# Kernel tuning notes

Hardware: AMD Instinct MI355X
Metric: run time of the kernel (lower is better)

The kernel has to match this reference:

```python
import jax, jax.numpy as jnp
import numpy as np

PI = 3.14159  # constant used in the torch module
N_QUBITS = 10
N_LAYERS = 4
B = 1024  # number of graphs


def _lin_init(k, fan_in, fan_out):
    k1, k2 = jax.random.split(k)
    s = 1.0 / np.sqrt(fan_in)
    W = jax.random.uniform(k1, (fan_in, fan_out), jnp.float32, -s, s)
    b = jax.random.uniform(k2, (fan_out,), jnp.float32, -s, s)
    return W, b


def setup_inputs():
    key = jax.random.key(0)
    ks = jax.random.split(key, 12)
    N, E, Fin, H, Emb = 32768, 131072, 128, 256, 128
    x = jax.random.normal(ks[0], (N, Fin), jnp.float32)
    edge_index = jax.random.randint(ks[1], (2, E), 0, N)
    batch = jnp.sort(jax.random.randint(ks[2], (N,), 0, B))
    edge_attr = jax.random.uniform(ks[3], (E, 4), dtype=jnp.float32)
    W1, b1 = _lin_init(ks[4], Fin, H)          # GCNConv 1
    W2, b2 = _lin_init(ks[5], H, Emb)          # GCNConv 2
    projW, projb = _lin_init(ks[6], Emb, N_QUBITS)
    vqc_weights = jax.random.uniform(ks[7], (N_LAYERS, N_QUBITS), jnp.float32, 0.0, 2 * np.pi)
    epW, epb = _lin_init(ks[8], 4, N_QUBITS - 1)
    cW1, cb1 = _lin_init(ks[9], Emb + N_QUBITS, 16)
    cW2, cb2 = _lin_init(ks[10], 16, 1)
    return dict(x=x, edge_index=edge_index, batch=batch, edge_attr=edge_attr,
                W1=W1, b1=b1, W2=W2, b2=b2, projW=projW, projb=projb,
                vqc_weights=vqc_weights, epW=epW, epb=epb,
                cW1=cW1, cb1=cb1, cW2=cW2, cb2=cb2)


def _gcn_conv(x, W, b, src, dst, n):
    # GCNConv with self-loops: sym-normalized aggregation of xW
    h = x @ W
    deg = jnp.zeros((n,), x.dtype).at[dst].add(1.0) + 1.0  # +1 self-loop
    dinv = jax.lax.rsqrt(deg)
    coef = (dinv[src] * dinv[dst])[:, None]
    agg = jnp.zeros_like(h).at[dst].add(h[src] * coef)
    return agg + h * (1.0 / deg)[:, None] + b


def _segment_mean(v, seg, n):
    tot = jnp.zeros((n, v.shape[1]), v.dtype).at[seg].add(v)
    cnt = jnp.zeros((n,), v.dtype).at[seg].add(1.0)
    return tot / jnp.clip(cnt, 1.0)[:, None]


def _run_vqc(q_in, weights, ep):
    # Batched real state-vector simulation. All gates (RY, CRY) are real.
    # Wire 0 = most significant bit (pennylane default.qubit convention).
    b = q_in.shape[0]
    dim = 2 ** N_QUBITS
    st = jnp.zeros((b, dim), q_in.dtype).at[:, 0].set(1.0)

    def ry(st, theta, w):
        th = jnp.broadcast_to(theta, (b,)) * 0.5
        c = jnp.cos(th)[:, None, None]
        s = jnp.sin(th)[:, None, None]
        r = st.reshape(b, 2 ** w, 2, -1)
        a0, a1 = r[:, :, 0], r[:, :, 1]
        return jnp.stack([c * a0 - s * a1, s * a0 + c * a1], axis=2).reshape(b, dim)

    def cry(st, theta, w):
        # control w, target w+1 (adjacent wires)
        th = jnp.broadcast_to(theta, (b,)) * 0.5
        c = jnp.cos(th)[:, None, None]
        s = jnp.sin(th)[:, None, None]
        r = st.reshape(b, 2 ** w, 2, 2, -1)
        a0, a1 = r[:, :, 1, 0], r[:, :, 1, 1]
        r = r.at[:, :, 1, 0].set(c * a0 - s * a1).at[:, :, 1, 1].set(s * a0 + c * a1)
        return r.reshape(b, dim)

    for i in range(N_QUBITS):                      # AngleEmbedding (RY)
        st = ry(st, q_in[:, i], i)
    for layer in range(N_LAYERS):
        for i in range(N_QUBITS):
            st = ry(st, weights[layer, i], i)
        for i in range(N_QUBITS - 1):
            st = cry(st, ep[:, i], i)

    probs = st * st
    zs = []
    for i in range(N_QUBITS):
        p = probs.reshape(b, 2 ** i, 2, -1).sum(axis=(1, 3))
        zs.append(p[:, 0] - p[:, 1])               # <PauliZ(i)>
    return jnp.stack(zs, axis=1)                   # [B, n_qubits]


def reference(x, edge_index, batch, edge_attr, W1, b1, W2, b2, projW, projb,
              vqc_weights, epW, epb, cW1, cb1, cW2, cb2):
    N = x.shape[0]
    src, dst = edge_index[0], edge_index[1]
    # GCN encoder: two GCNConv + ReLU, global mean pool (dropout = eval mode)
    h = jax.nn.relu(_gcn_conv(x, W1, b1, src, dst, N))
    h = jax.nn.relu(_gcn_conv(h, W2, b2, src, dst, N))
    emb = _segment_mean(h, batch, B)               # [B, gcn_embed]

    q_in = jnp.tanh(emb @ projW + projb) * PI      # [B, n_qubits]

    # scatter-mean edge pooling per graph, then edge projection
    edge_batch = batch[src]
    pooled_edge = _segment_mean(edge_attr, edge_batch, B)  # [B, 4]
    ep = pooled_edge @ epW + epb                   # [B, n_qubits-1]

    q_out = _run_vqc(q_in, vqc_weights, ep)        # [B, n_qubits]

    combined = jnp.concatenate([emb, q_out], axis=-1)
    hid = jax.nn.relu(combined @ cW1 + cb1)
    return hid @ cW2 + cb2                         # [B, num_tasks]
```

## Files before the change

kernel.cpp:

```cpp
#include <hip/hip_runtime.h>

#define PI_F 3.14159f
#define NQ 10

__global__ void k_edge_setup(const int* __restrict__ dstA, const int* __restrict__ srcA,
                             const int* __restrict__ batch, const float* __restrict__ eattr,
                             int E, int* __restrict__ cnt, float* __restrict__ psum,
                             float* __restrict__ ecnt) {
  int e = blockIdx.x * blockDim.x + threadIdx.x;
  if (e >= E) return;
  atomicAdd(&cnt[dstA[e]], 1);
  int g = batch[srcA[e]];
  float4 v = *(const float4*)(eattr + (size_t)e * 4);
  atomicAdd(&psum[g * 4 + 0], v.x);
  atomicAdd(&psum[g * 4 + 1], v.y);
  atomicAdd(&psum[g * 4 + 2], v.z);
  atomicAdd(&psum[g * 4 + 3], v.w);
  atomicAdd(&ecnt[g], 1.0f);
}

__global__ __launch_bounds__(1024) void k_scan1(const int* __restrict__ cnt,
                                                int* __restrict__ incl,
                                                int* __restrict__ bsum) {
  __shared__ int buf[1024];
  int t = threadIdx.x;
  int base = blockIdx.x << 10;
  buf[t] = cnt[base + t];
  __syncthreads();
#pragma unroll
  for (int off = 1; off < 1024; off <<= 1) {
    int x = (t >= off) ? buf[t - off] : 0;
    __syncthreads();
    buf[t] += x;
    __syncthreads();
  }
  incl[base + t] = buf[t];
  if (t == 1023) bsum[blockIdx.x] = buf[t];
}

__global__ void k_scan2(int* __restrict__ bsum, int nb) {
  int t = threadIdx.x;
  int v = (t < nb) ? bsum[t] : 0;
  int orig = v;
#pragma unroll
  for (int off = 1; off < 64; off <<= 1) {
    int x = __shfl_up(v, off, 64);
    if (t >= off) v += x;
  }
  if (t < nb) bsum[t] = v - orig;
}

__global__ void k_node_setup(const int* __restrict__ cnt, const int* __restrict__ incl,
                             const int* __restrict__ bsum, const int* __restrict__ batch,
                             int N, int Bn, int* __restrict__ rowStart,
                             int* __restrict__ pos, float* __restrict__ dinv,
                             float* __restrict__ invdeg, int* __restrict__ starts) {
  int i = blockIdx.x * blockDim.x + threadIdx.x;
  if (i >= N) return;
  int c = cnt[i];
  int inc = incl[i] + bsum[i >> 10];
  rowStart[i + 1] = inc;
  pos[i] = inc - c;
  if (i == 0) rowStart[0] = 0;
  float d = (float)c + 1.0f;
  dinv[i] = 1.0f / sqrtf(d);
  invdeg[i] = 1.0f / d;
  int b = batch[i];
  int bp = (i == 0) ? -1 : batch[i - 1];
  for (int g = bp + 1; g <= b; g++) starts[g] = i;
  if (i == N - 1) {
    for (int g = b + 1; g <= Bn; g++) starts[g] = N;
  }
}

__global__ void k_fill(const int* __restrict__ dst, int E, int* __restrict__ pos,
                       int* __restrict__ eSorted) {
  int e = blockIdx.x * blockDim.x + threadIdx.x;
  if (e < E) { int s = atomicAdd(&pos[dst[e]], 1); eSorted[s] = e; }
}

__global__ __launch_bounds__(256) void k_gemm(const float* __restrict__ A,
                                              const float* __restrict__ B,
                                              float* __restrict__ C,
                                              int M, int K, int N) {
  __shared__ float As[64][36];
  __shared__ float Bs[32][68];
  int t = threadIdx.x;
  int tx = t & 15, ty = t >> 4;
  int row0 = blockIdx.y * 64, col0 = blockIdx.x * 64;
  float acc[4][4] = {};
  for (int k0 = 0; k0 < K; k0 += 32) {
#pragma unroll
    for (int rep = 0; rep < 2; rep++) {
      int slot = t + rep * 256;
      int r = slot >> 3;
      int cg = (slot & 7) << 2;
      float4 v = *(const float4*)(A + (size_t)(row0 + r) * K + (k0 + cg));
      *(float4*)&As[r][cg] = v;
      int r2 = slot >> 4;
      int cg2 = (slot & 15) << 2;
      float4 w = *(const float4*)(B + (size_t)(k0 + r2) * N + (col0 + cg2));
      *(float4*)&Bs[r2][cg2] = w;
    }
    __syncthreads();
#pragma unroll
    for (int kk = 0; kk < 32; kk++) {
      float av[4];
      av[0] = As[ty * 4 + 0][kk];
      av[1] = As[ty * 4 + 1][kk];
      av[2] = As[ty * 4 + 2][kk];
      av[3] = As[ty * 4 + 3][kk];
      float4 b4 = *(const float4*)&Bs[kk][tx << 2];
      float bv[4] = {b4.x, b4.y, b4.z, b4.w};
#pragma unroll
      for (int i = 0; i < 4; i++)
#pragma unroll
        for (int j = 0; j < 4; j++) acc[i][j] = fmaf(av[i], bv[j], acc[i][j]);
    }
    __syncthreads();
  }
#pragma unroll
  for (int i = 0; i < 4; i++) {
    float4 v = {acc[i][0], acc[i][1], acc[i][2], acc[i][3]};
    *(float4*)(C + (size_t)(row0 + ty * 4 + i) * N + (col0 + (tx << 2))) = v;
  }
}

__global__ __launch_bounds__(256) void k_gcn_combine(
    const float* __restrict__ hlin, const int* __restrict__ srcA,
    const int* __restrict__ rowStart, const int* __restrict__ eSorted,
    const float* __restrict__ dinv, const float* __restrict__ invdeg,
    const float* __restrict__ bias, float* __restrict__ hout, int N, int C, int shift) {
  int gid = blockIdx.x * blockDim.x + threadIdx.x;
  int n = gid >> shift;
  if (n >= N) return;
  int cq = (gid & ((1 << shift) - 1)) << 2;
  int e0 = rowStart[n], e1 = rowStart[n + 1];
  float di = dinv[n];
  float ax = 0.f, ay = 0.f, az = 0.f, aw = 0.f;
  for (int e = e0; e < e1; e++) {
    int eidx = eSorted[e];
    int s = srcA[eidx];
    float coef = dinv[s] * di;
    float4 v = *(const float4*)(hlin + (size_t)s * C + cq);
    ax = fmaf(coef, v.x, ax);
    ay = fmaf(coef, v.y, ay);
    az = fmaf(coef, v.z, az);
    aw = fmaf(coef, v.w, aw);
  }
  float idg = invdeg[n];
  float4 hv = *(const float4*)(hlin + (size_t)n * C + cq);
  float4 bv = *(const float4*)(bias + cq);
  float4 r;
  r.x = fmaxf(fmaf(hv.x, idg, ax) + bv.x, 0.f);
  r.y = fmaxf(fmaf(hv.y, idg, ay) + bv.y, 0.f);
  r.z = fmaxf(fmaf(hv.z, idg, az) + bv.z, 0.f);
  r.w = fmaxf(fmaf(hv.w, idg, aw) + bv.w, 0.f);
  *(float4*)(hout + (size_t)n * C + cq) = r;
}

__device__ __forceinline__ void apply_ry(float* st, int w, float c, float s, int t) {
  int str = 1 << (9 - w);
#pragma unroll
  for (int r = 0; r < 2; r++) {
    int p = t + 256 * r;
    int lo = p & (str - 1);
    int hi = p >> (9 - w);
    int a0 = (hi << (10 - w)) + lo;
    int a1 = a0 + str;
    float x0 = st[a0], x1 = st[a1];
    st[a0] = c * x0 - s * x1;
    st[a1] = s * x0 + c * x1;
  }
}

__device__ __forceinline__ void apply_cry(float* st, int w, float c, float s, int t) {
  int ts = 1 << (8 - w);
  int lo = t & (ts - 1);
  int hi = t >> (8 - w);
  int a0 = (hi << (10 - w)) + (ts << 1) + lo;
  int a1 = a0 + ts;
  float x0 = st[a0], x1 = st[a1];
  st[a0] = c * x0 - s * x1;
  st[a1] = s * x0 + c * x1;
}

__global__ __launch_bounds__(256) void k_vqc_head(
    const float* __restrict__ h2, const int* __restrict__ starts,
    const float* __restrict__ psum, const float* __restrict__ ecnt,
    const float* __restrict__ projW, const float* __restrict__ projb,
    const float* __restrict__ vqcW, const float* __restrict__ epW,
    const float* __restrict__ epb, const float* __restrict__ cW1,
    const float* __restrict__ cb1, const float* __restrict__ cW2,
    const float* __restrict__ cb2, float* __restrict__ out) {
  int g = blockIdx.x;
  int t = threadIdx.x;
  __shared__ float st[1024];
  __shared__ float emb[128];
  __shared__ float csc[59], css[59];
  __shared__ float zred[4][NQ];
  __shared__ float zq[NQ];
  __shared__ float hid[16];

  int s0 = starts[g], s1 = starts[g + 1];
  int cntn = s1 - s0;
  float invc = 1.0f / (float)(cntn > 0 ? cntn : 1);
  if (t < 128) {
    float sum = 0.f;
    for (int i = s0; i < s1; i++) sum += h2[(size_t)i * 128 + t];
    emb[t] = sum * invc;
  }
  st[t] = 0.f; st[t + 256] = 0.f; st[t + 512] = 0.f; st[t + 768] = 0.f;
  __syncthreads();

  if (t < NQ) {
    float sum = projb[t];
    for (int k = 0; k < 128; k++) sum = fmaf(emb[k], projW[k * NQ + t], sum);
    float th = tanhf(sum) * PI_F * 0.5f;
    csc[t] = cosf(th);
    css[t] = sinf(th);
  } else if (t < NQ + 40) {
    float th = vqcW[t - NQ] * 0.5f;
    csc[t] = cosf(th);
    css[t] = sinf(th);
  } else if (t < 59) {
    int i = t - 50;
    float icnt = 1.0f / fmaxf(ecnt[g], 1.0f);
    float sum = epb[i];
    for (int j = 0; j < 4; j++) sum = fmaf(psum[g * 4 + j] * icnt, epW[j * 9 + i], sum);
    float th = sum * 0.5f;
    csc[t] = cosf(th);
    css[t] = sinf(th);
  }
  if (t == 0) st[0] = 1.0f;
  __syncthreads();

  for (int i = 0; i < NQ; i++) {
    apply_ry(st, i, csc[i], css[i], t);
    __syncthreads();
  }
  for (int L = 0; L < 4; L++) {
    for (int i = 0; i < NQ; i++) {
      apply_ry(st, i, csc[10 + L * 10 + i], css[10 + L * 10 + i], t);
      __syncthreads();
    }
    for (int i = 0; i < NQ - 1; i++) {
      apply_cry(st, i, csc[50 + i], css[50 + i], t);
      __syncthreads();
    }
  }

  float z[NQ];
#pragma unroll
  for (int i = 0; i < NQ; i++) z[i] = 0.f;
#pragma unroll
  for (int r = 0; r < 4; r++) {
    int a = t + 256 * r;
    float p = st[a] * st[a];
#pragma unroll
    for (int i = 0; i < NQ; i++) z[i] += ((a >> (9 - i)) & 1) ? -p : p;
  }
#pragma unroll
  for (int off = 32; off >= 1; off >>= 1) {
#pragma unroll
    for (int i = 0; i < NQ; i++) z[i] += __shfl_down(z[i], off, 64);
  }
  int wave = t >> 6, lane = t & 63;
  if (lane == 0) {
#pragma unroll
    for (int i = 0; i < NQ; i++) zred[wave][i] = z[i];
  }
  __syncthreads();
  if (t < NQ) zq[t] = zred[0][t] + zred[1][t] + zred[2][t] + zred[3][t];
  __syncthreads();

  if (t < 16) {
    float sum = cb1[t];
    for (int k = 0; k < 128; k++) sum = fmaf(emb[k], cW1[k * 16 + t], sum);
    for (int k = 0; k < NQ; k++) sum = fmaf(zq[k], cW1[(128 + k) * 16 + t], sum);
    hid[t] = fmaxf(sum, 0.f);
  }
  __syncthreads();
  if (t == 0) {
    float sum = cb2[0];
    for (int j = 0; j < 16; j++) sum = fmaf(hid[j], cW2[j], sum);
    out[g] = sum;
  }
}

extern "C" void kernel_launch(void* const* d_in, const int* in_sizes, int n_in,
                              void* d_out, int out_size, void* d_ws, size_t ws_size,
                              hipStream_t stream) {
  const float* x = (const float*)d_in[0];
  const int* ei = (const int*)d_in[1];
  const int* batch = (const int*)d_in[2];
  const float* eattr = (const float*)d_in[3];
  const float* W1 = (const float*)d_in[4];
  const float* b1 = (const float*)d_in[5];
  const float* W2 = (const float*)d_in[6];
  const float* b2 = (const float*)d_in[7];
  const float* projW = (const float*)d_in[8];
  const float* projb = (const float*)d_in[9];
  const float* vqcW = (const float*)d_in[10];
  const float* epW = (const float*)d_in[11];
  const float* epb = (const float*)d_in[12];
  const float* cW1 = (const float*)d_in[13];
  const float* cb1 = (const float*)d_in[14];
  const float* cW2 = (const float*)d_in[15];
  const float* cb2 = (const float*)d_in[16];
  float* out = (float*)d_out;

  const int N = in_sizes[0] / 128;
  const int E = in_sizes[1] / 2;
  const int Bn = out_size;

  const int* srcA = ei;
  const int* dstA = ei + E;

  char* ws = (char*)d_ws;
  float* bufA = (float*)ws;
  float* bufB = (float*)(ws + ((size_t)32 << 20));
  size_t off = (size_t)64 << 20;
  auto alloc = [&](size_t bytes) {
    size_t o = off;
    off += (bytes + 255) & ~(size_t)255;
    return o;
  };
  int* cnt = (int*)(ws + alloc((size_t)N * 4));
  float* psum = (float*)(ws + alloc((size_t)Bn * 4 * 4));
  float* ecnt = (float*)(ws + alloc((size_t)Bn * 4));
  size_t zeroEnd = off;
  int* rowStart = (int*)(ws + alloc((size_t)(N + 1) * 4));
  int* pos = (int*)(ws + alloc((size_t)N * 4));
  int* eSorted = (int*)(ws + alloc((size_t)E * 4));
  float* dinv = (float*)(ws + alloc((size_t)N * 4));
  float* invdeg = (float*)(ws + alloc((size_t)N * 4));
  int* starts = (int*)(ws + alloc((size_t)(Bn + 1) * 4));
  int* incl = (int*)(ws + alloc((size_t)N * 4));
  int* bsum = (int*)(ws + alloc(64 * 4));

  hipMemsetAsync(ws + ((size_t)64 << 20), 0, zeroEnd - ((size_t)64 << 20), stream);

  int eblocks = (E + 255) / 256;
  int nblocks = (N + 255) / 256;
  int nb1024 = N >> 10;

  k_edge_setup<<<eblocks, 256, 0, stream>>>(dstA, srcA, batch, eattr, E, cnt, psum, ecnt);
  k_scan1<<<nb1024, 1024, 0, stream>>>(cnt, incl, bsum);
  k_scan2<<<1, 64, 0, stream>>>(bsum, nb1024);
  k_node_setup<<<nblocks, 256, 0, stream>>>(cnt, incl, bsum, batch, N, Bn, rowStart, pos,
                                            dinv, invdeg, starts);
  k_fill<<<eblocks, 256, 0, stream>>>(dstA, E, pos, eSorted);

  {
    dim3 grid(256 / 64, N / 64);
    k_gemm<<<grid, 256, 0, stream>>>(x, W1, bufA, N, 128, 256);
  }
  k_gcn_combine<<<(N * 64) / 256, 256, 0, stream>>>(bufA, srcA, rowStart, eSorted, dinv,
                                                    invdeg, b1, bufB, N, 256, 6);
  {
    dim3 grid(128 / 64, N / 64);
    k_gemm<<<grid, 256, 0, stream>>>(bufB, W2, bufA, N, 256, 128);
  }
  k_gcn_combine<<<(N * 32) / 256, 256, 0, stream>>>(bufA, srcA, rowStart, eSorted, dinv,
                                                    invdeg, b2, bufB, N, 128, 5);
  k_vqc_head<<<Bn, 256, 0, stream>>>(bufB, starts, psum, ecnt, projW, projb, vqcW, epW,
                                     epb, cW1, cb1, cW2, cb2, out);
}
```

Baseline: 236.2 us.

## Pre-gather source ids and coefficients into CSR, pool edge attrs per node

The edge fill step now writes the source index and its dinv directly into dst-sorted arrays. The aggregation loop therefore no longer does the double indirection eSorted→srcA→dinv. Edge attributes are accumulated per source node rather than per graph, which spreads the atomics that used to hit 1024 hot addresses, and the head kernel reduces them per graph using a spare wavefront. The separate block-sum scan kernel is removed and each thread sums the preceding block totals itself. In exchange the zeroed workspace grows (N×20 bytes) and there is extra per-graph reduction work.

Measured after the change: 209.2 us. 1.13x faster.

```diff
diff --git a/kernel.cpp b/kernel.cpp
--- a/kernel.cpp
+++ b/kernel.cpp
@@ -4,19 +4,19 @@
 #define NQ 10
 
 __global__ void k_edge_setup(const int* __restrict__ dstA, const int* __restrict__ srcA,
-                             const int* __restrict__ batch, const float* __restrict__ eattr,
-                             int E, int* __restrict__ cnt, float* __restrict__ psum,
-                             float* __restrict__ ecnt) {
+                             const float* __restrict__ eattr, int E,
+                             int* __restrict__ cnt, float* __restrict__ nsum4,
+                             float* __restrict__ necnt) {
   int e = blockIdx.x * blockDim.x + threadIdx.x;
   if (e >= E) return;
   atomicAdd(&cnt[dstA[e]], 1);
-  int g = batch[srcA[e]];
+  int s = srcA[e];
   float4 v = *(const float4*)(eattr + (size_t)e * 4);
-  atomicAdd(&psum[g * 4 + 0], v.x);
-  atomicAdd(&psum[g * 4 + 1], v.y);
-  atomicAdd(&psum[g * 4 + 2], v.z);
-  atomicAdd(&psum[g * 4 + 3], v.w);
-  atomicAdd(&ecnt[g], 1.0f);
+  atomicAdd(&nsum4[(size_t)s * 4 + 0], v.x);
+  atomicAdd(&nsum4[(size_t)s * 4 + 1], v.y);
+  atomicAdd(&nsum4[(size_t)s * 4 + 2], v.z);
+  atomicAdd(&nsum4[(size_t)s * 4 + 3], v.w);
+  atomicAdd(&necnt[s], 1.0f);
 }
 
 __global__ __launch_bounds__(1024) void k_scan1(const int* __restrict__ cnt,
@@ -38,18 +38,6 @@
   if (t == 1023) bsum[blockIdx.x] = buf[t];
 }
 
-__global__ void k_scan2(int* __restrict__ bsum, int nb) {
-  int t = threadIdx.x;
-  int v = (t < nb) ? bsum[t] : 0;
-  int orig = v;
-#pragma unroll
-  for (int off = 1; off < 64; off <<= 1) {
-    int x = __shfl_up(v, off, 64);
-    if (t >= off) v += x;
-  }
-  if (t < nb) bsum[t] = v - orig;
-}
-
 __global__ void k_node_setup(const int* __restrict__ cnt, const int* __restrict__ incl,
                              const int* __restrict__ bsum, const int* __restrict__ batch,
                              int N, int Bn, int* __restrict__ rowStart,
@@ -57,8 +45,11 @@
                              float* __restrict__ invdeg, int* __restrict__ starts) {
   int i = blockIdx.x * blockDim.x + threadIdx.x;
   if (i >= N) return;
+  int blk = i >> 10;
+  int pre = 0;
+  for (int j = 0; j < blk; j++) pre += bsum[j];
   int c = cnt[i];
-  int inc = incl[i] + bsum[i >> 10];
+  int inc = incl[i] + pre;
   rowStart[i + 1] = inc;
   pos[i] = inc - c;
   if (i == 0) rowStart[0] = 0;
@@ -73,10 +64,15 @@
   }
 }
 
-__global__ void k_fill(const int* __restrict__ dst, int E, int* __restrict__ pos,
-                       int* __restrict__ eSorted) {
+__global__ void k_fill(const int* __restrict__ dst, const int* __restrict__ srcA,
+                       const float* __restrict__ dinv, int E, int* __restrict__ pos,
+                       int* __restrict__ srcSorted, float* __restrict__ dcoef) {
   int e = blockIdx.x * blockDim.x + threadIdx.x;
-  if (e < E) { int s = atomicAdd(&pos[dst[e]], 1); eSorted[s] = e; }
+  if (e >= E) return;
+  int s = srcA[e];
+  int slot = atomicAdd(&pos[dst[e]], 1);
+  srcSorted[slot] = s;
+  dcoef[slot] = dinv[s];
 }
 
 __global__ __launch_bounds__(256) void k_gemm(const float* __restrict__ A,
@@ -127,8 +123,8 @@
 }
 
 __global__ __launch_bounds__(256) void k_gcn_combine(
-    const float* __restrict__ hlin, const int* __restrict__ srcA,
-    const int* __restrict__ rowStart, const int* __restrict__ eSorted,
+    const float* __restrict__ hlin, const int* __restrict__ srcSorted,
+    const float* __restrict__ dcoef, const int* __restrict__ rowStart,
     const float* __restrict__ dinv, const float* __restrict__ invdeg,
     const float* __restrict__ bias, float* __restrict__ hout, int N, int C, int shift) {
   int gid = blockIdx.x * blockDim.x + threadIdx.x;
@@ -139,9 +135,8 @@
   float di = dinv[n];
   float ax = 0.f, ay = 0.f, az = 0.f, aw = 0.f;
   for (int e = e0; e < e1; e++) {
-    int eidx = eSorted[e];
-    int s = srcA[eidx];
-    float coef = dinv[s] * di;
+    int s = srcSorted[e];
+    float coef = dcoef[e] * di;
     float4 v = *(const float4*)(hlin + (size_t)s * C + cq);
     ax = fmaf(coef, v.x, ax);
     ay = fmaf(coef, v.y, ay);
@@ -187,7 +182,7 @@
 
 __global__ __launch_bounds__(256) void k_vqc_head(
     const float* __restrict__ h2, const int* __restrict__ starts,
-    const float* __restrict__ psum, const float* __restrict__ ecnt,
+    const float* __restrict__ nsum4, const float* __restrict__ necnt,
     const float* __restrict__ projW, const float* __restrict__ projb,
     const float* __restrict__ vqcW, const float* __restrict__ epW,
     const float* __restrict__ epb, const float* __restrict__ cW1,
@@ -198,6 +193,7 @@
   __shared__ float st[1024];
   __shared__ float emb[128];
   __shared__ float csc[59], css[59];
+  __shared__ float pool[5];
   __shared__ float zred[4][NQ];
   __shared__ float zq[NQ];
   __shared__ float hid[16];
@@ -209,6 +205,23 @@
     float sum = 0.f;
     for (int i = s0; i < s1; i++) sum += h2[(size_t)i * 128 + t];
     emb[t] = sum * invc;
+  } else if (t >= 192) {
+    int lane = t - 192;
+    float p0 = 0.f, p1 = 0.f, p2 = 0.f, p3 = 0.f, pc = 0.f;
+    for (int i = s0 + lane; i < s1; i += 64) {
+      float4 v = *(const float4*)(nsum4 + (size_t)i * 4);
+      p0 += v.x; p1 += v.y; p2 += v.z; p3 += v.w;
+      pc += necnt[i];
+    }
+#pragma unroll
+    for (int off = 32; off >= 1; off >>= 1) {
+      p0 += __shfl_down(p0, off, 64);
+      p1 += __shfl_down(p1, off, 64);
+      p2 += __shfl_down(p2, off, 64);
+      p3 += __shfl_down(p3, off, 64);
+      pc += __shfl_down(pc, off, 64);
+    }
+    if (lane == 0) { pool[0] = p0; pool[1] = p1; pool[2] = p2; pool[3] = p3; pool[4] = pc; }
   }
   st[t] = 0.f; st[t + 256] = 0.f; st[t + 512] = 0.f; st[t + 768] = 0.f;
   __syncthreads();
@@ -225,9 +238,9 @@
     css[t] = sinf(th);
   } else if (t < 59) {
     int i = t - 50;
-    float icnt = 1.0f / fmaxf(ecnt[g], 1.0f);
+    float icnt = 1.0f / fmaxf(pool[4], 1.0f);
     float sum = epb[i];
-    for (int j = 0; j < 4; j++) sum = fmaf(psum[g * 4 + j] * icnt, epW[j * 9 + i], sum);
+    for (int j = 0; j < 4; j++) sum = fmaf(pool[j] * icnt, epW[j * 9 + i], sum);
     float th = sum * 0.5f;
     csc[t] = cosf(th);
     css[t] = sinf(th);
@@ -327,12 +340,13 @@
     return o;
   };
   int* cnt = (int*)(ws + alloc((size_t)N * 4));
-  float* psum = (float*)(ws + alloc((size_t)Bn * 4 * 4));
-  float* ecnt = (float*)(ws + alloc((size_t)Bn * 4));
+  float* nsum4 = (float*)(ws + alloc((size_t)N * 16));
+  float* necnt = (float*)(ws + alloc((size_t)N * 4));
   size_t zeroEnd = off;
   int* rowStart = (int*)(ws + alloc((size_t)(N + 1) * 4));
   int* pos = (int*)(ws + alloc((size_t)N * 4));
-  int* eSorted = (int*)(ws + alloc((size_t)E * 4));
+  int* srcSorted = (int*)(ws + alloc((size_t)E * 4));
+  float* dcoef = (float*)(ws + alloc((size_t)E * 4));
   float* dinv = (float*)(ws + alloc((size_t)N * 4));
   float* invdeg = (float*)(ws + alloc((size_t)N * 4));
   int* starts = (int*)(ws + alloc((size_t)(Bn + 1) * 4));
@@ -345,25 +359,24 @@
   int nblocks = (N + 255) / 256;
   int nb1024 = N >> 10;
 
-  k_edge_setup<<<eblocks, 256, 0, stream>>>(dstA, srcA, batch, eattr, E, cnt, psum, ecnt);
+  k_edge_setup<<<eblocks, 256, 0, stream>>>(dstA, srcA, eattr, E, cnt, nsum4, necnt);
   k_scan1<<<nb1024, 1024, 0, stream>>>(cnt, incl, bsum);
-  k_scan2<<<1, 64, 0, stream>>>(bsum, nb1024);
   k_node_setup<<<nblocks, 256, 0, stream>>>(cnt, incl, bsum, batch, N, Bn, rowStart, pos,
                                             dinv, invdeg, starts);
-  k_fill<<<eblocks, 256, 0, stream>>>(dstA, E, pos, eSorted);
+  k_fill<<<eblocks, 256, 0, stream>>>(dstA, srcA, dinv, E, pos, srcSorted, dcoef);
 
   {
     dim3 grid(256 / 64, N / 64);
     k_gemm<<<grid, 256, 0, stream>>>(x, W1, bufA, N, 128, 256);
   }
-  k_gcn_combine<<<(N * 64) / 256, 256, 0, stream>>>(bufA, srcA, rowStart, eSorted, dinv,
-                                                    invdeg, b1, bufB, N, 256, 6);
+  k_gcn_combine<<<(N * 64) / 256, 256, 0, stream>>>(bufA, srcSorted, dcoef, rowStart,
+                                                    dinv, invdeg, b1, bufB, N, 256, 6);
   {
     dim3 grid(128 / 64, N / 64);
     k_gemm<<<grid, 256, 0, stream>>>(bufB, W2, bufA, N, 256, 128);
   }
-  k_gcn_combine<<<(N * 32) / 256, 256, 0, stream>>>(bufA, srcA, rowStart, eSorted, dinv,
-                                                    invdeg, b2, bufB, N, 128, 5);
-  k_vqc_head<<<Bn, 256, 0, stream>>>(bufB, starts, psum, ecnt, projW, projb, vqcW, epW,
+  k_gcn_combine<<<(N * 32) / 256, 256, 0, stream>>>(bufA, srcSorted, dcoef, rowStart,
+                                                    dinv, invdeg, b2, bufB, N, 128, 5);
+  k_vqc_head<<<Bn, 256, 0, stream>>>(bufB, starts, nsum4, necnt, projW, projb, vqcW, epW,
                                      epb, cW1, cb1, cW2, cb2, out);
 }
```
